# Optimization experiments

Measured on AMD Instinct MI355X. Metric: run time of the kernel, lower is better.

## Reference

```python
import jax, jax.numpy as jnp
import numpy as np

B, N, M = 4, 1024, 2048
D, H, HD, L, V = 768, 6, 128, 3, 4096
PEH = 64
FF = 4 * D
TEMP0 = 15.5


def _rms(x, w):
    return x * jax.lax.rsqrt(jnp.mean(x * x, axis=-1, keepdims=True) + 1e-8) * w


def _l2(x):
    n = jnp.sqrt(jnp.sum(x * x, axis=-1, keepdims=True))
    return x / jnp.maximum(n, 1e-12)


def setup_inputs():
    key = jax.random.key(0)
    it = iter(jax.random.split(key, 32))

    def rn(shape, s=0.02):
        return jax.random.normal(next(it), shape, jnp.float32) * s

    inp = {}
    inp['tokens'] = jax.random.randint(next(it), (B, N), 0, V)
    inp['acoustic'] = jax.random.normal(next(it), (B, M, D), jnp.float32)
    inp['embed'] = rn((V, D))
    inp['pe_freq'] = rn((PEH // 2,), 1.0)
    inp['pe_w'] = rn((PEH, D))
    inp['pe_b'] = jnp.zeros((D,), jnp.float32)
    inp['dpb_w0'] = rn((1, 64), 0.5)
    inp['dpb_b0'] = jnp.zeros((64,), jnp.float32)
    inp['dpb_w1'] = rn((64, 64), 0.1)
    inp['dpb_b1'] = jnp.zeros((64,), jnp.float32)
    inp['dpb_w2'] = rn((64, H), 0.1)
    inp['dpb_b2'] = jnp.zeros((H,), jnp.float32)
    inp['acoustic_norm_w'] = jnp.ones((D,), jnp.float32)
    inp['norm1'] = jnp.ones((L, D), jnp.float32)
    inp['norm2'] = jnp.ones((L, D), jnp.float32)
    inp['norm3'] = jnp.ones((L, D), jnp.float32)
    inp['sa_qkv'] = rn((L, D, 3 * H * HD))
    inp['sa_out'] = rn((L, H * HD, D))
    inp['temp'] = jnp.full((L,), TEMP0, jnp.float32)
    inp['ca_q'] = rn((L, D, H * HD))
    inp['ca_kv'] = rn((L, D, 2 * H * HD))
    inp['ca_out'] = rn((L, H * HD, D))
    inp['ff_w1'] = rn((L, D, FF))
    inp['ff_w2'] = rn((L, FF, D))
    inp['final_norm_w'] = jnp.ones((D,), jnp.float32)
    inp['out_w'] = rn((D, V))
    inp['out_b'] = jnp.zeros((V,), jnp.float32)
    return inp


def reference(tokens, acoustic, embed, pe_freq, pe_w, pe_b, dpb_w0, dpb_b0, dpb_w1, dpb_b1, dpb_w2, dpb_b2, acoustic_norm_w, norm1, norm2, norm3, sa_qkv, sa_out, temp, ca_q, ca_kv, ca_out, ff_w1, ff_w2, final_norm_w, out_w, out_b):
    x = embed[tokens]  # [B,N,D]
    # learnable fourier positional encoding (hidden_dim=64)
    p = jnp.arange(N, dtype=jnp.float32)[:, None]
    feat = jnp.concatenate([jnp.cos(p * pe_freq), jnp.sin(p * pe_freq)], axis=-1) / jnp.sqrt(jnp.float32(PEH))
    x = x + (feat @ pe_w + pe_b)

    # DynamicPositionBias: MLP over relative distance -> [H,N,N]
    dist = jnp.arange(-(N - 1), N, dtype=jnp.float32)[:, None]  # [2N-1,1]
    hmlp = jax.nn.silu(dist @ dpb_w0 + dpb_b0)
    hmlp = jax.nn.silu(hmlp @ dpb_w1 + dpb_b1)
    table = hmlp @ dpb_w2 + dpb_b2  # [2N-1, H]
    i = jnp.arange(N)
    rel = i[None, :] - i[:, None] + (N - 1)  # [N,N]
    pos_bias = jnp.transpose(table[rel], (2, 0, 1))  # [H,N,N]
    causal = i[None, :] > i[:, None]  # True where key index > query index
    neg = -jnp.finfo(jnp.float32).max

    xkv = _rms(acoustic, acoustic_norm_w)  # acoustic_norm applied once

    for l in range(L):
        # --- cosine-sim causal self-attention with temperature + pos bias ---
        hx = _rms(x, norm1[l])
        qkv = (hx @ sa_qkv[l]).reshape(B, N, H, HD, 3)  # 'b n (h d qkv)'
        q = jnp.transpose(qkv[..., 0], (0, 2, 1, 3))  # [B,H,N,HD]
        k = jnp.transpose(qkv[..., 1], (0, 2, 1, 3))
        v = jnp.transpose(qkv[..., 2], (0, 2, 1, 3))
        q, k = _l2(q), _l2(k)
        dots = jnp.einsum('bhid,bhjd->bhij', q, k) * temp[l] + pos_bias
        dots = jnp.where(causal, neg, dots)
        attn = jax.nn.softmax(dots, axis=-1)
        o = jnp.einsum('bhij,bhjd->bhid', attn, v)
        o = jnp.transpose(o, (0, 2, 1, 3)).reshape(B, N, H * HD)
        x = x + o @ sa_out[l]

        # --- cross attention to acoustic features (flash-attn math, scale 1/sqrt(d)) ---
        hx = _rms(x, norm2[l])
        q = (hx @ ca_q[l]).reshape(B, N, H, HD)
        kv = (xkv @ ca_kv[l]).reshape(B, M, H, HD, 2)  # 'b n (h d kv)'
        k, v = kv[..., 0], kv[..., 1]
        dots = jnp.einsum('bihd,bjhd->bhij', q, k) / jnp.sqrt(jnp.float32(HD))
        attn = jax.nn.softmax(dots, axis=-1)
        o = jnp.einsum('bhij,bjhd->bihd', attn, v).reshape(B, N, H * HD)
        x = x + o @ ca_out[l]

        # --- feed-forward: linear -> gelu -> linear ---
        hx = _rms(x, norm3[l])
        x = x + jax.nn.gelu(hx @ ff_w1[l], approximate=True) @ ff_w2[l]

    logits = _rms(x, final_norm_w) @ out_w + out_b  # [B,N,V]
    return logits
```

## Files before the change

kernel.cpp:

```cpp
#include <hip/hip_runtime.h>
#include <hip/hip_bf16.h>
#include <math.h>
#include <stddef.h>

#define Bc 4
#define Nc 1024
#define Mc 2048
#define Dc 768
#define Hc 6
#define HDc 128
#define Lc 3
#define Vc 4096
#define FFc 3072

typedef short bf16x8 __attribute__((ext_vector_type(8)));
typedef float f32x4 __attribute__((ext_vector_type(4)));
typedef ushort usx4 __attribute__((ext_vector_type(4)));

__device__ __forceinline__ float gelu_tanh(float x) {
    float x3 = x * x * x;
    return 0.5f * x * (1.0f + tanhf(0.7978845608028654f * (x + 0.044715f * x3)));
}
__device__ __forceinline__ float silu_f(float x) {
    return x / (1.0f + expf(-x));
}
__device__ __forceinline__ ushort f2bf(float x) {
    unsigned u = __float_as_uint(x);
    unsigned r = (u + 0x7fffu + ((u >> 16) & 1u)) >> 16;
    return (ushort)r;
}
__device__ __forceinline__ float bf2f(ushort u) {
    return __uint_as_float(((unsigned)u) << 16);
}
__device__ __forceinline__ void gl2lds16(const ushort* g, ushort* l) {
    __builtin_amdgcn_global_load_lds(
        (const __attribute__((address_space(1))) unsigned int*)(g),
        (__attribute__((address_space(3))) unsigned int*)(l),
        16, 0, 0);
}

__global__ __launch_bounds__(256) void pos_pe_kernel(
    const float* __restrict__ freq, const float* __restrict__ pe_w,
    const float* __restrict__ pe_b, float* __restrict__ pos)
{
    int n = blockIdx.x;
    __shared__ float feat[64];
    int tid = threadIdx.x;
    if (tid < 64) {
        float f;
        if (tid < 32) f = cosf((float)n * freq[tid]);
        else          f = sinf((float)n * freq[tid - 32]);
        feat[tid] = f * 0.125f;
    }
    __syncthreads();
    for (int d = tid; d < Dc; d += 256) {
        float s = pe_b[d];
#pragma unroll
        for (int h = 0; h < 64; ++h) s += feat[h] * pe_w[h * Dc + d];
        pos[(size_t)n * Dc + d] = s;
    }
}

__global__ __launch_bounds__(256) void embed_kernel(
    const int* __restrict__ tokens, const float* __restrict__ embed_w,
    const float* __restrict__ pos, float* __restrict__ x)
{
    size_t idx = (size_t)blockIdx.x * 256 + threadIdx.x;
    if (idx >= (size_t)Bc * Nc * Dc) return;
    int d  = (int)(idx % Dc);
    size_t bn = idx / Dc;
    int n  = (int)(bn % Nc);
    int tok = tokens[bn];
    x[idx] = embed_w[(size_t)tok * Dc + d] + pos[(size_t)n * Dc + d];
}

__global__ __launch_bounds__(64) void dpb_kernel(
    const float* __restrict__ w0, const float* __restrict__ b0,
    const float* __restrict__ w1, const float* __restrict__ b1,
    const float* __restrict__ w2, const float* __restrict__ b2,
    float* __restrict__ table)
{
    int r = blockIdx.x;
    int j = threadIdx.x;
    float dist = (float)r - (float)(Nc - 1);
    __shared__ float s0[64], s1[64];
    s0[j] = silu_f(dist * w0[j] + b0[j]);
    __syncthreads();
    float a = b1[j];
#pragma unroll 8
    for (int k = 0; k < 64; ++k) a += s0[k] * w1[k * 64 + j];
    s1[j] = silu_f(a);
    __syncthreads();
    if (j < Hc) {
        float t = b2[j];
#pragma unroll 8
        for (int k = 0; k < 64; ++k) t += s1[k] * w2[k * Hc + j];
        table[(size_t)r * Hc + j] = t;
    }
}

__global__ __launch_bounds__(256) void rms_kernel(
    const float* __restrict__ in, const float* __restrict__ w,
    ushort* __restrict__ out)
{
    size_t row = blockIdx.x;
    const float* rp = in + row * Dc;
    ushort* op = out + row * Dc;
    int tid = threadIdx.x;
    float s = 0.f;
    for (int d = tid; d < Dc; d += 256) { float v = rp[d]; s += v * v; }
    __shared__ float red[256];
    red[tid] = s;
    __syncthreads();
    for (int o = 128; o > 0; o >>= 1) {
        if (tid < o) red[tid] += red[tid + o];
        __syncthreads();
    }
    float rs = rsqrtf(red[0] * (1.0f / Dc) + 1e-8f);
    for (int d = tid; d < Dc; d += 256) op[d] = f2bf(rp[d] * rs * w[d]);
}

__global__ __launch_bounds__(256) void wt_kernel(
    const float* __restrict__ in, ushort* __restrict__ out, int K_, int N_)
{
    int n0 = blockIdx.x << 6, k0 = blockIdx.y << 6;
    __shared__ ushort t[64][65];
    int tid = threadIdx.x;
    int r = tid >> 4, c4 = (tid & 15) << 2;
    for (int rr = r; rr < 64; rr += 16) {
        float4 v = *(const float4*)&in[(size_t)(k0 + rr) * N_ + n0 + c4];
        t[rr][c4]     = f2bf(v.x);
        t[rr][c4 + 1] = f2bf(v.y);
        t[rr][c4 + 2] = f2bf(v.z);
        t[rr][c4 + 3] = f2bf(v.w);
    }
    __syncthreads();
    int nr = tid >> 2, cw = (tid & 3) << 4;
    ushort tmp[16];
#pragma unroll
    for (int j = 0; j < 16; ++j) tmp[j] = t[cw + j][nr];
#pragma unroll
    for (int s = 0; s < 2; ++s)
        *(bf16x8*)&out[(size_t)(n0 + nr) * K_ + k0 + cw + (s << 3)] =
            *(const bf16x8*)&tmp[s << 3];
}

__global__ __launch_bounds__(256) void gemm_bf16_kernel(
    const ushort* __restrict__ A, const ushort* __restrict__ Bt,
    const float* __restrict__ bias, const float* __restrict__ res,
    float* __restrict__ Cf, ushort* __restrict__ Cb,
    int M_, int N_, int K_, int act)
{
    __shared__ __align__(16) ushort As[8 * 512];
    __shared__ __align__(16) ushort Bs[8 * 512];
    int m0 = blockIdx.y << 7, n0 = blockIdx.x << 7;
    int tid = threadIdx.x;
    int wave = tid >> 6, lane = tid & 63;
    int li = lane & 15, lq = lane >> 4;
    int wm = (wave >> 1) << 6, wn = (wave & 1) << 6;

    f32x4 acc[4][4];
#pragma unroll
    for (int i = 0; i < 4; ++i)
#pragma unroll
        for (int j = 0; j < 4; ++j) {
            acc[i][j][0] = 0.f; acc[i][j][1] = 0.f;
            acc[i][j][2] = 0.f; acc[i][j][3] = 0.f;
        }

    for (int k0 = 0; k0 < K_; k0 += 32) {
#pragma unroll
        for (int i = 0; i < 2; ++i) {
            int fb = (wave << 1) + i;
            const ushort* ga = A  + (size_t)(m0 + (fb << 4) + li) * K_ + k0 + (lq << 3);
            const ushort* gb = Bt + (size_t)(n0 + (fb << 4) + li) * K_ + k0 + (lq << 3);
            gl2lds16(ga, &As[fb << 9]);
            gl2lds16(gb, &Bs[fb << 9]);
        }
        __syncthreads();
        bf16x8 af[4], bfr[4];
#pragma unroll
        for (int t = 0; t < 4; ++t) {
            af[t]  = *(const bf16x8*)&As[(((wm >> 4) + t) << 9) + (lane << 3)];
            bfr[t] = *(const bf16x8*)&Bs[(((wn >> 4) + t) << 9) + (lane << 3)];
        }
#pragma unroll
        for (int mt = 0; mt < 4; ++mt)
#pragma unroll
            for (int nt = 0; nt < 4; ++nt)
                acc[mt][nt] = __builtin_amdgcn_mfma_f32_16x16x32_bf16(
                    af[mt], bfr[nt], acc[mt][nt], 0, 0, 0);
        __syncthreads();
    }

#pragma unroll
    for (int mt = 0; mt < 4; ++mt) {
#pragma unroll
        for (int r = 0; r < 4; ++r) {
            int row = m0 + wm + (mt << 4) + (lq << 2) + r;
#pragma unroll
            for (int nt = 0; nt < 4; ++nt) {
                int col = n0 + wn + (nt << 4) + li;
                float v = acc[mt][nt][r];
                if (bias) v += bias[col];
                if (act == 1) v = gelu_tanh(v);
                if (res) v += res[(size_t)row * N_ + col];
                if (Cb) Cb[(size_t)row * N_ + col] = f2bf(v);
                else    Cf[(size_t)row * N_ + col] = v;
            }
        }
    }
}

__global__ __launch_bounds__(128) void unpack_sa_kernel(
    const ushort* __restrict__ qkv, ushort* __restrict__ qo,
    ushort* __restrict__ ko, ushort* __restrict__ vo)
{
    int bid = blockIdx.x;
    int h = bid % Hc;
    int bn = bid / Hc;
    int b = bn / Nc, n = bn % Nc;
    int d = threadIdx.x;
    size_t base = (size_t)bn * (3 * Hc * HDc) + (size_t)(h * HDc + d) * 3;
    float q = bf2f(qkv[base]), k = bf2f(qkv[base + 1]);
    ushort v = qkv[base + 2];
    __shared__ float rq[128], rk[128];
    rq[d] = q * q; rk[d] = k * k;
    __syncthreads();
    for (int o = 64; o > 0; o >>= 1) {
        if (d < o) { rq[d] += rq[d + o]; rk[d] += rk[d + o]; }
        __syncthreads();
    }
    float qn = fmaxf(sqrtf(rq[0]), 1e-12f);
    float kn = fmaxf(sqrtf(rk[0]), 1e-12f);
    size_t oidx = (((size_t)(b * Hc + h) * Nc) + n) * HDc + d;
    qo[oidx] = f2bf(q / qn);
    ko[oidx] = f2bf(k / kn);
    vo[oidx] = v;
}

__global__ __launch_bounds__(256) void unpack_caq_kernel(
    const ushort* __restrict__ in, ushort* __restrict__ qo)
{
    size_t idx = (size_t)blockIdx.x * 256 + threadIdx.x;
    if (idx >= (size_t)Bc * Hc * Nc * HDc) return;
    int d = (int)(idx & (HDc - 1));
    size_t t = idx >> 7;
    int n = (int)(t % Nc); t /= Nc;
    int h = (int)(t % Hc); int b = (int)(t / Hc);
    qo[idx] = in[((size_t)(b * Nc + n)) * (Hc * HDc) + h * HDc + d];
}

__global__ __launch_bounds__(256) void unpack_cakv_kernel(
    const ushort* __restrict__ in, ushort* __restrict__ ko, ushort* __restrict__ vo)
{
    size_t idx = (size_t)blockIdx.x * 256 + threadIdx.x;
    if (idx >= (size_t)Bc * Hc * Mc * HDc) return;
    int d = (int)(idx & (HDc - 1));
    size_t t = idx >> 7;
    int m = (int)(t % Mc); t /= Mc;
    int h = (int)(t % Hc); int b = (int)(t / Hc);
    size_t src = ((size_t)(b * Mc + m)) * (2 * Hc * HDc) + (size_t)(h * HDc + d) * 2;
    ko[idx] = in[src];
    vo[idx] = in[src + 1];
}

__global__ __launch_bounds__(256) void transpose_kernel(
    const ushort* __restrict__ in, ushort* __restrict__ out, int R)
{
    int bh = blockIdx.z;
    int r0 = blockIdx.x << 6, d0 = blockIdx.y << 6;
    const ushort* ip = in + (size_t)bh * R * HDc;
    ushort* op = out + (size_t)bh * HDc * R;
    __shared__ ushort tile[64][66];
    int t = threadIdx.x;
    int lr = t >> 5, lc = (t & 31) << 1;
    for (int rr = lr; rr < 64; rr += 8) {
        ushort2 v = *(const ushort2*)&ip[(size_t)(r0 + rr) * HDc + d0 + lc];
        tile[rr][lc] = v.x; tile[rr][lc + 1] = v.y;
    }
    __syncthreads();
    for (int dd = lr; dd < 64; dd += 8) {
        ushort2 v;
        v.x = tile[lc][dd]; v.y = tile[lc + 1][dd];
        *(ushort2*)&op[(size_t)(d0 + dd) * R + r0 + lc] = v;
    }
}

__global__ __launch_bounds__(256) void attn_mfma_kernel(
    const ushort* __restrict__ Qg, const ushort* __restrict__ Kg,
    const ushort* __restrict__ VTg, ushort* __restrict__ O,
    int NQ, int NK, float scale_const, const float* __restrict__ scale_ptr,
    const float* __restrict__ bias_table, int causal)
{
    int qtiles = NQ >> 6;
    int qt = blockIdx.x % qtiles;
    int bh = blockIdx.x / qtiles;
    int h = bh % Hc, b = bh / Hc;
    int q0 = qt << 6;

    const ushort* Qb = Qg + (size_t)bh * NQ * HDc;
    const ushort* Kb = Kg + (size_t)bh * NK * HDc;
    const ushort* Vb = VTg + (size_t)bh * HDc * NK;

    float scale = scale_const * (scale_ptr ? scale_ptr[0] : 1.0f);

    __shared__ __align__(16) ushort Ks[16 * 512];
    __shared__ __align__(16) ushort Vs[16 * 512];
    __shared__ __align__(16) ushort Ps[4][16][72];
    __shared__ float bias_s[128];

    int tid = threadIdx.x;
    int wave = tid >> 6, lane = tid & 63;
    int li = lane & 15, lq = lane >> 4;
    int qrel = (wave << 4) + li;

    bf16x8 qfrag[4];
    {
        const ushort* qrow = Qb + (size_t)(q0 + qrel) * HDc + (lq << 3);
#pragma unroll
        for (int kt = 0; kt < 4; ++kt)
            qfrag[kt] = *(const bf16x8*)&qrow[kt << 5];
    }

    f32x4 oacc[8];
#pragma unroll
    for (int i = 0; i < 8; ++i) { oacc[i][0] = 0.f; oacc[i][1] = 0.f; oacc[i][2] = 0.f; oacc[i][3] = 0.f; }
    float m_run = -INFINITY, l_run = 0.f;

    int jt_end = causal ? (q0 >> 6) + 1 : (NK >> 6);
    for (int jt = 0; jt < jt_end; ++jt) {
        int j0 = jt << 6;
#pragma unroll
        for (int i = 0; i < 4; ++i) {
            int f = (wave << 2) + i;
            int mt = f >> 2, kt = f & 3;
            const ushort* gk = Kb + (size_t)(j0 + (mt << 4) + li) * HDc + (kt << 5) + (lq << 3);
            gl2lds16(gk, &Ks[f << 9]);
            int dt = f >> 1, s = f & 1;
            const ushort* gv = Vb + (size_t)((dt << 4) + li) * NK + j0 + (s << 5) + (lq << 3);
            gl2lds16(gv, &Vs[f << 9]);
        }
        if (bias_table && tid < 127)
            bias_s[tid] = bias_table[(size_t)(j0 - q0 - 63 + Nc - 1 + tid) * Hc + h];
        __syncthreads();

        f32x4 sacc[4];
#pragma unroll
        for (int mt = 0; mt < 4; ++mt) {
            f32x4 s; s[0] = 0.f; s[1] = 0.f; s[2] = 0.f; s[3] = 0.f;
#pragma unroll
            for (int kt = 0; kt < 4; ++kt) {
                bf16x8 kf = *(const bf16x8*)&Ks[(((mt << 2) + kt) << 9) + (lane << 3)];
                s = __builtin_amdgcn_mfma_f32_16x16x32_bf16(kf, qfrag[kt], s, 0, 0, 0);
            }
            sacc[mt] = s;
        }

        float sv[4][4];
        float mtile = -INFINITY;
#pragma unroll
        for (int mt = 0; mt < 4; ++mt)
#pragma unroll
            for (int r = 0; r < 4; ++r) {
                int jrel = (mt << 4) + (lq << 2) + r;
                float sx = sacc[mt][r] * scale;
                if (bias_table) sx += bias_s[jrel - qrel + 63];
                if (causal && (j0 + jrel) > (q0 + qrel)) sx = -INFINITY;
                sv[mt][r] = sx;
                mtile = fmaxf(mtile, sx);
            }
        mtile = fmaxf(mtile, __shfl_xor(mtile, 16));
        mtile = fmaxf(mtile, __shfl_xor(mtile, 32));
        float m_new = fmaxf(m_run, mtile);
        float alpha = __expf(m_run - m_new);
        m_run = m_new;
        float ps = 0.f;
#pragma unroll
        for (int mt = 0; mt < 4; ++mt)
#pragma unroll
            for (int r = 0; r < 4; ++r) {
                float p = __expf(sv[mt][r] - m_new);
                sv[mt][r] = p;
                ps += p;
            }
        ps += __shfl_xor(ps, 16);
        ps += __shfl_xor(ps, 32);
        l_run = l_run * alpha + ps;

#pragma unroll
        for (int mt = 0; mt < 4; ++mt) {
            usx4 pk;
            pk.x = f2bf(sv[mt][0]); pk.y = f2bf(sv[mt][1]);
            pk.z = f2bf(sv[mt][2]); pk.w = f2bf(sv[mt][3]);
            *(usx4*)&Ps[wave][li][(mt << 4) + (lq << 2)] = pk;
        }

        float ar[4];
#pragma unroll
        for (int r = 0; r < 4; ++r) ar[r] = __shfl(alpha, (lq << 2) + r);
#pragma unroll
        for (int dt = 0; dt < 8; ++dt)
#pragma unroll
            for (int r = 0; r < 4; ++r) oacc[dt][r] *= ar[r];

        bf16x8 pf0 = *(const bf16x8*)&Ps[wave][li][(lq << 3)];
        bf16x8 pf1 = *(const bf16x8*)&Ps[wave][li][32 + (lq << 3)];
#pragma unroll
        for (int dt = 0; dt < 8; ++dt) {
            bf16x8 v0 = *(const bf16x8*)&Vs[(((dt << 1) + 0) << 9) + (lane << 3)];
            bf16x8 v1 = *(const bf16x8*)&Vs[(((dt << 1) + 1) << 9) + (lane << 3)];
            oacc[dt] = __builtin_amdgcn_mfma_f32_16x16x32_bf16(pf0, v0, oacc[dt], 0, 0, 0);
            oacc[dt] = __builtin_amdgcn_mfma_f32_16x16x32_bf16(pf1, v1, oacc[dt], 0, 0, 0);
        }
        __syncthreads();
    }

#pragma unroll
    for (int r = 0; r < 4; ++r) {
        float linv = 1.0f / __shfl(l_run, (lq << 2) + r);
        int gq = q0 + (wave << 4) + (lq << 2) + r;
        ushort* op = O + ((size_t)(b * NQ + gq)) * (Hc * HDc) + h * HDc;
#pragma unroll
        for (int dt = 0; dt < 8; ++dt)
            op[(dt << 4) + li] = f2bf(oacc[dt][r] * linv);
    }
}

static inline void launch_gemm(const ushort* A, const ushort* Bt, const float* bias,
                               const float* res, float* Cf, ushort* Cb,
                               int M_, int N_, int K_, int act, hipStream_t s)
{
    dim3 g(N_ / 128, M_ / 128);
    hipLaunchKernelGGL(gemm_bf16_kernel, g, dim3(256), 0, s,
                       A, Bt, bias, res, Cf, Cb, M_, N_, K_, act);
}

extern "C" void kernel_launch(void* const* d_in, const int* in_sizes, int n_in,
                              void* d_out, int out_size, void* d_ws, size_t ws_size,
                              hipStream_t stream)
{
    const int*   tokens   = (const int*)  d_in[0];
    const float* acoustic = (const float*)d_in[1];
    const float* embed_w  = (const float*)d_in[2];
    const float* pe_freq  = (const float*)d_in[3];
    const float* pe_w     = (const float*)d_in[4];
    const float* pe_b     = (const float*)d_in[5];
    const float* dpb_w0   = (const float*)d_in[6];
    const float* dpb_b0   = (const float*)d_in[7];
    const float* dpb_w1   = (const float*)d_in[8];
    const float* dpb_b1   = (const float*)d_in[9];
    const float* dpb_w2   = (const float*)d_in[10];
    const float* dpb_b2   = (const float*)d_in[11];
    const float* ac_nw    = (const float*)d_in[12];
    const float* norm1    = (const float*)d_in[13];
    const float* norm2    = (const float*)d_in[14];
    const float* norm3    = (const float*)d_in[15];
    const float* sa_qkv   = (const float*)d_in[16];
    const float* sa_out_w = (const float*)d_in[17];
    const float* temp     = (const float*)d_in[18];
    const float* ca_q_w   = (const float*)d_in[19];
    const float* ca_kv_w  = (const float*)d_in[20];
    const float* ca_out_w = (const float*)d_in[21];
    const float* ff_w1    = (const float*)d_in[22];
    const float* ff_w2    = (const float*)d_in[23];
    const float* fin_nw   = (const float*)d_in[24];
    const float* out_w    = (const float*)d_in[25];
    const float* out_b    = (const float*)d_in[26];
    float* out = (float*)d_out;

    const size_t SZ_X   = (size_t)Bc * Nc * Dc;
    const size_t SZ_POS = (size_t)Nc * Dc;
    const size_t SZ_TAB = 16384;
    const size_t SZ_XKV = (size_t)Bc * Mc * Dc;
    const size_t SZ_BIG = (size_t)Bc * Nc * FFc;
    const size_t SZ_QH  = (size_t)Bc * Hc * Nc * HDc;
    const size_t SZ_KH  = (size_t)Bc * Hc * Mc * HDc;

    float* ws = (float*)d_ws;
    float* x     = ws;
    float* pos   = x + SZ_X;
    float* table = pos + SZ_POS;
    ushort* hx    = (ushort*)(table + SZ_TAB);
    ushort* xkvb  = hx + SZ_X;
    ushort* attnO = xkvb + SZ_XKV;
    ushort* bigBb = attnO + SZ_X;
    ushort* qb    = bigBb + SZ_BIG;
    ushort* kb    = qb + SZ_QH;
    ushort* vb    = kb + SZ_KH;
    ushort* vTb   = vb + SZ_KH;
    ushort* wT    = vTb + SZ_KH;

    const size_t W_QKV = (size_t)Dc * 3 * Hc * HDc;
    const size_t W_O   = (size_t)Hc * HDc * Dc;
    const size_t W_CKV = (size_t)Dc * 2 * Hc * HDc;
    const size_t W_F   = (size_t)Dc * FFc;
    const size_t W_LAYER = W_QKV + 3 * W_O + W_CKV + 2 * W_F;
    ushort* outWT = wT + 3 * W_LAYER;

    const float CA_SCALE = 0.08838834764831843f;

    for (int l = 0; l < Lc; ++l) {
        ushort* wl = wT + (size_t)l * W_LAYER;
        ushort* qkvT = wl;
        ushort* soT  = qkvT + W_QKV;
        ushort* cqT  = soT + W_O;
        ushort* ckvT = cqT + W_O;
        ushort* coT  = ckvT + W_CKV;
        ushort* f1T  = coT + W_O;
        ushort* f2T  = f1T + W_F;
        hipLaunchKernelGGL(wt_kernel, dim3(3 * Hc * HDc / 64, Dc / 64), dim3(256), 0, stream,
                           sa_qkv + (size_t)l * W_QKV, qkvT, Dc, 3 * Hc * HDc);
        hipLaunchKernelGGL(wt_kernel, dim3(Dc / 64, Hc * HDc / 64), dim3(256), 0, stream,
                           sa_out_w + (size_t)l * W_O, soT, Hc * HDc, Dc);
        hipLaunchKernelGGL(wt_kernel, dim3(Hc * HDc / 64, Dc / 64), dim3(256), 0, stream,
                           ca_q_w + (size_t)l * W_O, cqT, Dc, Hc * HDc);
        hipLaunchKernelGGL(wt_kernel, dim3(2 * Hc * HDc / 64, Dc / 64), dim3(256), 0, stream,
                           ca_kv_w + (size_t)l * W_CKV, ckvT, Dc, 2 * Hc * HDc);
        hipLaunchKernelGGL(wt_kernel, dim3(Dc / 64, Hc * HDc / 64), dim3(256), 0, stream,
                           ca_out_w + (size_t)l * W_O, coT, Hc * HDc, Dc);
        hipLaunchKernelGGL(wt_kernel, dim3(FFc / 64, Dc / 64), dim3(256), 0, stream,
                           ff_w1 + (size_t)l * W_F, f1T, Dc, FFc);
        hipLaunchKernelGGL(wt_kernel, dim3(Dc / 64, FFc / 64), dim3(256), 0, stream,
                           ff_w2 + (size_t)l * W_F, f2T, FFc, Dc);
    }
    hipLaunchKernelGGL(wt_kernel, dim3(Vc / 64, Dc / 64), dim3(256), 0, stream,
                       out_w, outWT, Dc, Vc);

    hipLaunchKernelGGL(pos_pe_kernel, dim3(Nc), dim3(256), 0, stream,
                       pe_freq, pe_w, pe_b, pos);
    hipLaunchKernelGGL(embed_kernel, dim3((unsigned)((SZ_X + 255) / 256)), dim3(256), 0, stream,
                       tokens, embed_w, pos, x);
    hipLaunchKernelGGL(dpb_kernel, dim3(2 * Nc - 1), dim3(64), 0, stream,
                       dpb_w0, dpb_b0, dpb_w1, dpb_b1, dpb_w2, dpb_b2, table);
    hipLaunchKernelGGL(rms_kernel, dim3(Bc * Mc), dim3(256), 0, stream,
                       acoustic, ac_nw, xkvb);

    for (int l = 0; l < Lc; ++l) {
        const float* n1 = norm1 + (size_t)l * Dc;
        const float* n2 = norm2 + (size_t)l * Dc;
        const float* n3 = norm3 + (size_t)l * Dc;
        ushort* wl = wT + (size_t)l * W_LAYER;
        ushort* qkvT = wl;
        ushort* soT  = qkvT + W_QKV;
        ushort* cqT  = soT + W_O;
        ushort* ckvT = cqT + W_O;
        ushort* coT  = ckvT + W_CKV;
        ushort* f1T  = coT + W_O;
        ushort* f2T  = f1T + W_F;

        hipLaunchKernelGGL(rms_kernel, dim3(Bc * Nc), dim3(256), 0, stream, x, n1, hx);
        launch_gemm(hx, qkvT, nullptr, nullptr, nullptr, bigBb,
                    Bc * Nc, 3 * Hc * HDc, Dc, 0, stream);
        hipLaunchKernelGGL(unpack_sa_kernel, dim3(Bc * Nc * Hc), dim3(128), 0, stream,
                           bigBb, qb, kb, vb);
        hipLaunchKernelGGL(transpose_kernel, dim3(Nc / 64, 2, Bc * Hc), dim3(256), 0, stream,
                           vb, vTb, Nc);
        hipLaunchKernelGGL(attn_mfma_kernel, dim3(Bc * Hc * (Nc / 64)), dim3(256), 0, stream,
                           qb, kb, vTb, attnO, Nc, Nc, 1.0f, temp + l, table, 1);
        launch_gemm(attnO, soT, nullptr, x, x, nullptr,
                    Bc * Nc, Dc, Hc * HDc, 0, stream);

        hipLaunchKernelGGL(rms_kernel, dim3(Bc * Nc), dim3(256), 0, stream, x, n2, hx);
        launch_gemm(hx, cqT, nullptr, nullptr, nullptr, bigBb,
                    Bc * Nc, Hc * HDc, Dc, 0, stream);
        hipLaunchKernelGGL(unpack_caq_kernel, dim3((unsigned)((SZ_QH + 255) / 256)), dim3(256),
                           0, stream, bigBb, qb);
        launch_gemm(xkvb, ckvT, nullptr, nullptr, nullptr, bigBb,
                    Bc * Mc, 2 * Hc * HDc, Dc, 0, stream);
        hipLaunchKernelGGL(unpack_cakv_kernel, dim3((unsigned)((SZ_KH + 255) / 256)), dim3(256),
                           0, stream, bigBb, kb, vb);
        hipLaunchKernelGGL(transpose_kernel, dim3(Mc / 64, 2, Bc * Hc), dim3(256), 0, stream,
                           vb, vTb, Mc);
        hipLaunchKernelGGL(attn_mfma_kernel, dim3(Bc * Hc * (Nc / 64)), dim3(256), 0, stream,
                           qb, kb, vTb, attnO, Nc, Mc, CA_SCALE, nullptr, nullptr, 0);
        launch_gemm(attnO, coT, nullptr, x, x, nullptr,
                    Bc * Nc, Dc, Hc * HDc, 0, stream);

        hipLaunchKernelGGL(rms_kernel, dim3(Bc * Nc), dim3(256), 0, stream, x, n3, hx);
        launch_gemm(hx, f1T, nullptr, nullptr, nullptr, bigBb,
                    Bc * Nc, FFc, Dc, 1, stream);
        launch_gemm(bigBb, f2T, nullptr, x, x, nullptr,
                    Bc * Nc, Dc, FFc, 0, stream);
    }

    hipLaunchKernelGGL(rms_kernel, dim3(Bc * Nc), dim3(256), 0, stream, x, fin_nw, hx);
    launch_gemm(hx, outWT, out_b, nullptr, out, nullptr,
                Bc * Nc, Vc, Dc, 0, stream);
}
```

Baseline: 2.214 ms.

## Double-buffer LDS in GEMM and attention; split-K residual GEMMs with atomics

Adds double-buffered LDS staging to both the GEMM and flash-attention kernels, so the next tile's global-to-LDS loads are issued before the current tile's MFMAs, cutting the barrier-separated load/compute serialization. It also introduces split-K for the residual-add GEMMs (out-projections with split 2, FF2 with split 4), which accumulate directly into x with float atomicAdd. That raises block count for the narrow N=768 GEMMs. The costs are doubled LDS use, which may lower occupancy, atomic traffic, and non-deterministic summation order.

```diff
diff --git a/kernel.cpp b/kernel.cpp
--- a/kernel.cpp
+++ b/kernel.cpp
@@ -149,16 +149,20 @@
     const ushort* __restrict__ A, const ushort* __restrict__ Bt,
     const float* __restrict__ bias, const float* __restrict__ res,
     float* __restrict__ Cf, ushort* __restrict__ Cb,
-    int M_, int N_, int K_, int act)
-{
-    __shared__ __align__(16) ushort As[8 * 512];
-    __shared__ __align__(16) ushort Bs[8 * 512];
+    int M_, int N_, int K_, int act, int ksplit)
+{
+    __shared__ __align__(16) ushort As[2][8 * 512];
+    __shared__ __align__(16) ushort Bs[2][8 * 512];
     int m0 = blockIdx.y << 7, n0 = blockIdx.x << 7;
     int tid = threadIdx.x;
     int wave = tid >> 6, lane = tid & 63;
     int li = lane & 15, lq = lane >> 4;
     int wm = (wave >> 1) << 6, wn = (wave & 1) << 6;
 
+    int kchunk = K_ / ksplit;
+    int kbeg = blockIdx.z * kchunk;
+    int niter = kchunk >> 5;
+
     f32x4 acc[4][4];
 #pragma unroll
     for (int i = 0; i < 4; ++i)
@@ -168,21 +172,28 @@
             acc[i][j][2] = 0.f; acc[i][j][3] = 0.f;
         }
 
-    for (int k0 = 0; k0 < K_; k0 += 32) {
+    auto stage = [&](int buf, int k0) {
 #pragma unroll
         for (int i = 0; i < 2; ++i) {
             int fb = (wave << 1) + i;
             const ushort* ga = A  + (size_t)(m0 + (fb << 4) + li) * K_ + k0 + (lq << 3);
             const ushort* gb = Bt + (size_t)(n0 + (fb << 4) + li) * K_ + k0 + (lq << 3);
-            gl2lds16(ga, &As[fb << 9]);
-            gl2lds16(gb, &Bs[fb << 9]);
-        }
-        __syncthreads();
+            gl2lds16(ga, &As[buf][fb << 9]);
+            gl2lds16(gb, &Bs[buf][fb << 9]);
+        }
+    };
+
+    stage(0, kbeg);
+    __syncthreads();
+
+    for (int it = 0; it < niter; ++it) {
+        int cur = it & 1;
+        if (it + 1 < niter) stage(cur ^ 1, kbeg + ((it + 1) << 5));
         bf16x8 af[4], bfr[4];
 #pragma unroll
         for (int t = 0; t < 4; ++t) {
-            af[t]  = *(const bf16x8*)&As[(((wm >> 4) + t) << 9) + (lane << 3)];
-            bfr[t] = *(const bf16x8*)&Bs[(((wn >> 4) + t) << 9) + (lane << 3)];
+            af[t]  = *(const bf16x8*)&As[cur][(((wm >> 4) + t) << 9) + (lane << 3)];
+            bfr[t] = *(const bf16x8*)&Bs[cur][(((wn >> 4) + t) << 9) + (lane << 3)];
         }
 #pragma unroll
         for (int mt = 0; mt < 4; ++mt)
@@ -191,6 +202,22 @@
                 acc[mt][nt] = __builtin_amdgcn_mfma_f32_16x16x32_bf16(
                     af[mt], bfr[nt], acc[mt][nt], 0, 0, 0);
         __syncthreads();
+    }
+
+    if (ksplit > 1) {
+#pragma unroll
+        for (int mt = 0; mt < 4; ++mt) {
+#pragma unroll
+            for (int r = 0; r < 4; ++r) {
+                int row = m0 + wm + (mt << 4) + (lq << 2) + r;
+#pragma unroll
+                for (int nt = 0; nt < 4; ++nt) {
+                    int col = n0 + wn + (nt << 4) + li;
+                    atomicAdd(&Cf[(size_t)row * N_ + col], acc[mt][nt][r]);
+                }
+            }
+        }
+        return;
     }
 
 #pragma unroll
@@ -305,10 +332,10 @@
 
     float scale = scale_const * (scale_ptr ? scale_ptr[0] : 1.0f);
 
-    __shared__ __align__(16) ushort Ks[16 * 512];
-    __shared__ __align__(16) ushort Vs[16 * 512];
+    __shared__ __align__(16) ushort Ks[2][16 * 512];
+    __shared__ __align__(16) ushort Vs[2][16 * 512];
     __shared__ __align__(16) ushort Ps[4][16][72];
-    __shared__ float bias_s[128];
+    __shared__ float bias_s[2][128];
 
     int tid = threadIdx.x;
     int wave = tid >> 6, lane = tid & 63;
@@ -328,22 +355,31 @@
     for (int i = 0; i < 8; ++i) { oacc[i][0] = 0.f; oacc[i][1] = 0.f; oacc[i][2] = 0.f; oacc[i][3] = 0.f; }
     float m_run = -INFINITY, l_run = 0.f;
 
-    int jt_end = causal ? (q0 >> 6) + 1 : (NK >> 6);
-    for (int jt = 0; jt < jt_end; ++jt) {
+    auto stage_kv = [&](int buf, int jt) {
         int j0 = jt << 6;
 #pragma unroll
         for (int i = 0; i < 4; ++i) {
             int f = (wave << 2) + i;
             int mt = f >> 2, kt = f & 3;
             const ushort* gk = Kb + (size_t)(j0 + (mt << 4) + li) * HDc + (kt << 5) + (lq << 3);
-            gl2lds16(gk, &Ks[f << 9]);
+            gl2lds16(gk, &Ks[buf][f << 9]);
             int dt = f >> 1, s = f & 1;
             const ushort* gv = Vb + (size_t)((dt << 4) + li) * NK + j0 + (s << 5) + (lq << 3);
-            gl2lds16(gv, &Vs[f << 9]);
+            gl2lds16(gv, &Vs[buf][f << 9]);
         }
         if (bias_table && tid < 127)
-            bias_s[tid] = bias_table[(size_t)(j0 - q0 - 63 + Nc - 1 + tid) * Hc + h];
-        __syncthreads();
+            bias_s[buf][tid] = bias_table[(size_t)(j0 - q0 - 63 + Nc - 1 + tid) * Hc + h];
+    };
+
+    int jt_end = causal ? (q0 >> 6) + 1 : (NK >> 6);
+
+    stage_kv(0, 0);
+    __syncthreads();
+
+    for (int jt = 0; jt < jt_end; ++jt) {
+        int cur = jt & 1;
+        if (jt + 1 < jt_end) stage_kv(cur ^ 1, jt + 1);
+        int j0 = jt << 6;
 
         f32x4 sacc[4];
 #pragma unroll
@@ -351,7 +387,7 @@
             f32x4 s; s[0] = 0.f; s[1] = 0.f; s[2] = 0.f; s[3] = 0.f;
 #pragma unroll
             for (int kt = 0; kt < 4; ++kt) {
-                bf16x8 kf = *(const bf16x8*)&Ks[(((mt << 2) + kt) << 9) + (lane << 3)];
+                bf16x8 kf = *(const bf16x8*)&Ks[cur][(((mt << 2) + kt) << 9) + (lane << 3)];
                 s = __builtin_amdgcn_mfma_f32_16x16x32_bf16(kf, qfrag[kt], s, 0, 0, 0);
             }
             sacc[mt] = s;
@@ -365,7 +401,7 @@
             for (int r = 0; r < 4; ++r) {
                 int jrel = (mt << 4) + (lq << 2) + r;
                 float sx = sacc[mt][r] * scale;
-                if (bias_table) sx += bias_s[jrel - qrel + 63];
+                if (bias_table) sx += bias_s[cur][jrel - qrel + 63];
                 if (causal && (j0 + jrel) > (q0 + qrel)) sx = -INFINITY;
                 sv[mt][r] = sx;
                 mtile = fmaxf(mtile, sx);
@@ -408,8 +444,8 @@
         bf16x8 pf1 = *(const bf16x8*)&Ps[wave][li][32 + (lq << 3)];
 #pragma unroll
         for (int dt = 0; dt < 8; ++dt) {
-            bf16x8 v0 = *(const bf16x8*)&Vs[(((dt << 1) + 0) << 9) + (lane << 3)];
-            bf16x8 v1 = *(const bf16x8*)&Vs[(((dt << 1) + 1) << 9) + (lane << 3)];
+            bf16x8 v0 = *(const bf16x8*)&Vs[cur][(((dt << 1) + 0) << 9) + (lane << 3)];
+            bf16x8 v1 = *(const bf16x8*)&Vs[cur][(((dt << 1) + 1) << 9) + (lane << 3)];
             oacc[dt] = __builtin_amdgcn_mfma_f32_16x16x32_bf16(pf0, v0, oacc[dt], 0, 0, 0);
             oacc[dt] = __builtin_amdgcn_mfma_f32_16x16x32_bf16(pf1, v1, oacc[dt], 0, 0, 0);
         }
@@ -429,11 +465,12 @@
 
 static inline void launch_gemm(const ushort* A, const ushort* Bt, const float* bias,
                                const float* res, float* Cf, ushort* Cb,
-                               int M_, int N_, int K_, int act, hipStream_t s)
-{
-    dim3 g(N_ / 128, M_ / 128);
+                               int M_, int N_, int K_, int act, int ksplit,
+                               hipStream_t s)
+{
+    dim3 g(N_ / 128, M_ / 128, ksplit);
     hipLaunchKernelGGL(gemm_bf16_kernel, g, dim3(256), 0, s,
-                       A, Bt, bias, res, Cf, Cb, M_, N_, K_, act);
+                       A, Bt, bias, res, Cf, Cb, M_, N_, K_, act, ksplit);
 }
 
 extern "C" void kernel_launch(void* const* d_in, const int* in_sizes, int n_in,
@@ -551,40 +588,40 @@
 
         hipLaunchKernelGGL(rms_kernel, dim3(Bc * Nc), dim3(256), 0, stream, x, n1, hx);
         launch_gemm(hx, qkvT, nullptr, nullptr, nullptr, bigBb,
-                    Bc * Nc, 3 * Hc * HDc, Dc, 0, stream);
+                    Bc * Nc, 3 * Hc * HDc, Dc, 0, 1, stream);
         hipLaunchKernelGGL(unpack_sa_kernel, dim3(Bc * Nc * Hc), dim3(128), 0, stream,
                            bigBb, qb, kb, vb);
         hipLaunchKernelGGL(transpose_kernel, dim3(Nc / 64, 2, Bc * Hc), dim3(256), 0, stream,
                            vb, vTb, Nc);
         hipLaunchKernelGGL(attn_mfma_kernel, dim3(Bc * Hc * (Nc / 64)), dim3(256), 0, stream,
                            qb, kb, vTb, attnO, Nc, Nc, 1.0f, temp + l, table, 1);
-        launch_gemm(attnO, soT, nullptr, x, x, nullptr,
-                    Bc * Nc, Dc, Hc * HDc, 0, stream);
+        launch_gemm(attnO, soT, nullptr, nullptr, x, nullptr,
+                    Bc * Nc, Dc, Hc * HDc, 0, 2, stream);
 
         hipLaunchKernelGGL(rms_kernel, dim3(Bc * Nc), dim3(256), 0, stream, x, n2, hx);
         launch_gemm(hx, cqT, nullptr, nullptr, nullptr, bigBb,
-                    Bc * Nc, Hc * HDc, Dc, 0, stream);
+                    Bc * Nc, Hc * HDc, Dc, 0, 1, stream);
         hipLaunchKernelGGL(unpack_caq_kernel, dim3((unsigned)((SZ_QH + 255) / 256)), dim3(256),
                            0, stream, bigBb, qb);
         launch_gemm(xkvb, ckvT, nullptr, nullptr, nullptr, bigBb,
-                    Bc * Mc, 2 * Hc * HDc, Dc, 0, stream);
+                    Bc * Mc, 2 * Hc * HDc, Dc, 0, 1, stream);
         hipLaunchKernelGGL(unpack_cakv_kernel, dim3((unsigned)((SZ_KH + 255) / 256)), dim3(256),
                            0, stream, bigBb, kb, vb);
         hipLaunchKernelGGL(transpose_kernel, dim3(Mc / 64, 2, Bc * Hc), dim3(256), 0, stream,
                            vb, vTb, Mc);
         hipLaunchKernelGGL(attn_mfma_kernel, dim3(Bc * Hc * (Nc / 64)), dim3(256), 0, stream,
                            qb, kb, vTb, attnO, Nc, Mc, CA_SCALE, nullptr, nullptr, 0);
-        launch_gemm(attnO, coT, nullptr, x, x, nullptr,
-                    Bc * Nc, Dc, Hc * HDc, 0, stream);
+        launch_gemm(attnO, coT, nullptr, nullptr, x, nullptr,
+                    Bc * Nc, Dc, Hc * HDc, 0, 2, stream);
 
         hipLaunchKernelGGL(rms_kernel, dim3(Bc * Nc), dim3(256), 0, stream, x, n3, hx);
         launch_gemm(hx, f1T, nullptr, nullptr, nullptr, bigBb,
-                    Bc * Nc, FFc, Dc, 1, stream);
-        launch_gemm(bigBb, f2T, nullptr, x, x, nullptr,
-                    Bc * Nc, Dc, FFc, 0, stream);
+                    Bc * Nc, FFc, Dc, 1, 1, stream);
+        launch_gemm(bigBb, f2T, nullptr, nullptr, x, nullptr,
+                    Bc * Nc, Dc, FFc, 0, 4, stream);
     }
 
     hipLaunchKernelGGL(rms_kernel, dim3(Bc * Nc), dim3(256), 0, stream, x, fin_nw, hx);
     launch_gemm(hx, outWT, out_b, nullptr, out, nullptr,
-                Bc * Nc, Vc, Dc, 0, stream);
-}
+                Bc * Nc, Vc, Dc, 0, 1, stream);
+}
```

Measured after the change: 1.940 ms. 12.4% less time.
